# Kernel optimization log

Measured on AMD Instinct MI355X. Metric: run time of the kernel, lower is better.

## Reference

```python
import jax, jax.numpy as jnp
import numpy as np

N_NODES = 50000
N_EDGES = 800000
D = 256
N_GRAPHS = 128
N_CLASSES = 2


def gcn_conv(x, W, b, src, dst, ew):
    # PyG GCNConv: add self-loops (weight 1), symmetric norm D^-1/2 (A+I) D^-1/2, then X@W + b
    n = x.shape[0]
    deg = jax.ops.segment_sum(ew, dst, num_segments=n) + 1.0  # includes self-loop weight
    dinv = jnp.where(deg > 0, jax.lax.rsqrt(deg), 0.0)
    xw = x @ W  # [N, D_out]
    norm = dinv[src] * ew * dinv[dst]  # [E]
    msgs = xw[src] * norm[:, None]  # [E, D_out] gathered messages
    agg = jax.ops.segment_sum(msgs, dst, num_segments=n)
    agg = agg + xw * (dinv * dinv)[:, None]  # self-loop contribution
    return agg + b


def setup_inputs() -> dict:
    key = jax.random.key(0)
    ks = jax.random.split(key, 16)
    emb_x = jax.random.normal(ks[0], (N_NODES, D), dtype=jnp.float32)
    edge_index = jax.random.randint(ks[1], (2, N_EDGES), 0, N_NODES, dtype=jnp.int64)
    edge_weight = jax.random.uniform(ks[2], (N_EDGES,), dtype=jnp.float32)
    batch = jnp.sort(jax.random.randint(ks[3], (N_NODES,), 0, N_GRAPHS, dtype=jnp.int64))
    s = 1.0 / np.sqrt(D)
    params = {}
    for i, k in enumerate(ks[4:7]):
        params[f"W{i+1}"] = jax.random.normal(k, (D, D), dtype=jnp.float32) * s
        params[f"b{i+1}"] = jnp.zeros((D,), dtype=jnp.float32)
    params["fc1_w"] = jax.random.normal(ks[7], (2 * D, D), dtype=jnp.float32) / np.sqrt(2 * D)
    params["fc1_b"] = jnp.zeros((D,), dtype=jnp.float32)
    params["fc2_w"] = jax.random.normal(ks[8], (D, N_CLASSES), dtype=jnp.float32) * s
    params["fc2_b"] = jnp.zeros((N_CLASSES,), dtype=jnp.float32)
    return dict(emb_x=emb_x, edge_index=edge_index, edge_weight=edge_weight, batch=batch, **params)


def reference(emb_x, edge_index, edge_weight, batch, W1, b1, W2, b2, W3, b3, fc1_w, fc1_b, fc2_w, fc2_b):
    src, dst = edge_index[0], edge_index[1]
    x = emb_x
    for W, b in ((W1, b1), (W2, b2), (W3, b3)):
        x = gcn_conv(x, W, b, src, dst, edge_weight)
        x = jax.nn.relu(x)  # dropout is identity in eval mode
    counts = jax.ops.segment_sum(jnp.ones((x.shape[0],), x.dtype), batch, num_segments=N_GRAPHS)
    mean_x = jax.ops.segment_sum(x, batch, num_segments=N_GRAPHS) / jnp.maximum(counts, 1.0)[:, None]
    max_x = jax.ops.segment_max(x, batch, num_segments=N_GRAPHS)
    max_x = jnp.where(jnp.isfinite(max_x), max_x, 0.0)  # empty segments -> 0
    h = jnp.concatenate([mean_x, max_x], axis=1)  # [G, 2D]
    h = jax.nn.relu(h @ fc1_w + fc1_b)
    return h @ fc2_w + fc2_b  # [G, n_classes]
```

## Files before the change

kernel.cpp:

```cpp
#include <hip/hip_runtime.h>
#include <math.h>

#define N_NODES 50000
#define N_PAD 50048
#define N_EDGES 800000
#define DIM 256
#define N_GRAPHS 128

using f32x4 = __attribute__((ext_vector_type(4))) float;
using s16x8 = __attribute__((ext_vector_type(8))) short;

__device__ __forceinline__ ushort bf16_hi(float f) {
  unsigned u = __float_as_uint(f);
  return (ushort)((u + 0x7FFFu + ((u >> 16) & 1u)) >> 16);
}
__device__ __forceinline__ float bf16_up(ushort h) {
  return __uint_as_float(((unsigned)h) << 16);
}
__device__ __forceinline__ void bf16_split(float f, ushort& hh, ushort& ll) {
  hh = bf16_hi(f);
  float d = f - bf16_up(hh);
  ll = bf16_hi(d);
}

__global__ __launch_bounds__(256) void count_kernel(
    const int* __restrict__ dst, int* __restrict__ counts,
    int* __restrict__ p_local) {
  int e = blockIdx.x * 256 + threadIdx.x;
  if (e < N_EDGES) p_local[e] = atomicAdd(&counts[dst[e]], 1);
}

#define SCAN_CHUNK 1024
#define SCAN_BLOCKS ((N_NODES + SCAN_CHUNK - 1) / SCAN_CHUNK)

__global__ __launch_bounds__(256) void scan_phaseA(
    const int* __restrict__ counts, int* __restrict__ blockSums) {
  __shared__ int sdata[256];
  int b = blockIdx.x, t = threadIdx.x;
  int base = b * SCAN_CHUNK + t * 4;
  int s = 0;
#pragma unroll
  for (int i = 0; i < 4; ++i) {
    int idx = base + i;
    if (idx < N_NODES) s += counts[idx];
  }
  sdata[t] = s;
  __syncthreads();
  for (int off = 128; off > 0; off >>= 1) {
    if (t < off) sdata[t] += sdata[t + off];
    __syncthreads();
  }
  if (t == 0) blockSums[b] = sdata[0];
}

__global__ void scan_phaseB(int* __restrict__ blockSums, int* __restrict__ rs) {
  if (threadIdx.x == 0 && blockIdx.x == 0) {
    int acc = 0;
    for (int i = 0; i < SCAN_BLOCKS; ++i) {
      int v = blockSums[i];
      blockSums[i] = acc;
      acc += v;
    }
    rs[N_NODES] = acc;
  }
}

__global__ __launch_bounds__(256) void scan_phaseC(
    const int* __restrict__ counts, const int* __restrict__ blockSums,
    int* __restrict__ rs) {
  __shared__ int sdata[256];
  int b = blockIdx.x, t = threadIdx.x;
  int base = b * SCAN_CHUNK + t * 4;
  int v[4];
  int s = 0;
#pragma unroll
  for (int i = 0; i < 4; ++i) {
    int idx = base + i;
    v[i] = (idx < N_NODES) ? counts[idx] : 0;
    s += v[i];
  }
  sdata[t] = s;
  __syncthreads();
  for (int off = 1; off < 256; off <<= 1) {
    int x = (t >= off) ? sdata[t - off] : 0;
    __syncthreads();
    sdata[t] += x;
    __syncthreads();
  }
  int excl = (t == 0) ? 0 : sdata[t - 1];
  int o = blockSums[b] + excl;
#pragma unroll
  for (int i = 0; i < 4; ++i) {
    int idx = base + i;
    if (idx < N_NODES) rs[idx] = o;
    o += v[i];
  }
}

__global__ __launch_bounds__(256) void fill_kernel(
    const int* __restrict__ src, const int* __restrict__ dst,
    const float* __restrict__ ew, const int* __restrict__ rs,
    const int* __restrict__ p_local,
    int* __restrict__ csrc, float* __restrict__ cw) {
  int e = blockIdx.x * 256 + threadIdx.x;
  if (e < N_EDGES) {
    int d = dst[e];
    int pos = rs[d] + p_local[e];
    csrc[pos] = src[e];
    cw[pos] = ew[e];
  }
}

__global__ __launch_bounds__(256) void degsum_kernel(
    const int* __restrict__ rs, const float* __restrict__ cw,
    float* __restrict__ dinv) {
  int n = blockIdx.x * 256 + threadIdx.x;
  if (n >= N_NODES) return;
  int b = rs[n], e = rs[n + 1];
  float s = 1.0f;
  for (int i = b; i < e; ++i) s += cw[i];
  dinv[n] = 1.0f / sqrtf(s);
}

__global__ __launch_bounds__(256) void norm_kernel(
    const int* __restrict__ csrc, const float* __restrict__ dinv,
    float* __restrict__ cw) {
  int e = blockIdx.x * 256 + threadIdx.x;
  if (e < N_EDGES) cw[e] = cw[e] * dinv[csrc[e]];
}

__global__ __launch_bounds__(256) void round_x_kernel(
    const float* __restrict__ x, ushort* __restrict__ tab, int n4) {
  int i = blockIdx.x * 256 + threadIdx.x;
  if (i >= n4) return;
  float4 v = ((const float4*)x)[i];
  ushort4 h;
  h.x = bf16_hi(v.x);
  h.y = bf16_hi(v.y);
  h.z = bf16_hi(v.z);
  h.w = bf16_hi(v.w);
  ((ushort4*)tab)[i] = h;
}

__global__ __launch_bounds__(256) void prep_w_kernel(
    const float* __restrict__ W1, const float* __restrict__ W2, const float* __restrict__ W3,
    ushort* __restrict__ wt) {
  int k = blockIdx.x;
  int w = blockIdx.y;
  int n = threadIdx.x;
  const float* W = (w == 0) ? W1 : (w == 1) ? W2 : W3;
  float v = W[k * 256 + n];
  ushort h, l;
  bf16_split(v, h, l);
  ushort* hplane = wt + (size_t)w * 2 * 256 * 256;
  ushort* lplane = hplane + 256 * 256;
  hplane[n * 256 + k] = h;
  lplane[n * 256 + k] = l;
}

#define GBM 64
#define GBK 32

__device__ __forceinline__ void gload16(const void* g, void* l) {
  __builtin_amdgcn_global_load_lds(
      (const __attribute__((address_space(1))) void*)g,
      (__attribute__((address_space(3))) void*)l, 16, 0, 0);
}

__global__ __launch_bounds__(256) void gemm_mfma(
    const ushort* __restrict__ A,
    const ushort* __restrict__ Wh, const ushort* __restrict__ Wl,
    ushort* __restrict__ C, int M) {
  __shared__ ushort Asl[2][GBM * GBK];
  int tid = threadIdx.x;
  int bm = blockIdx.x * GBM;
  int wave = tid >> 6, lane = tid & 63;
  int wc = wave * 64;
  int l15 = lane & 15;
  int lkb = lane >> 4;

  f32x4 acc[4][4];
#pragma unroll
  for (int i = 0; i < 4; ++i)
#pragma unroll
    for (int j = 0; j < 4; ++j) acc[i][j] = (f32x4){0.f, 0.f, 0.f, 0.f};

  int arow = tid & 63, akb = tid >> 6;

#define STAGE_A(buf, ts)                                                       \
  gload16(A + (size_t)(bm + arow) * 256 + (ts) * 32 + akb * 8,                 \
          &Asl[buf][tid * 8])

  STAGE_A(0, 0);
  s16x8 bh_c[4], bl_c[4], bh_n[4], bl_n[4];
#pragma unroll
  for (int f = 0; f < 4; ++f) {
    size_t woff = (size_t)(wc + f * 16 + l15) * 256 + lkb * 8;
    bh_c[f] = *(const s16x8*)(Wh + woff);
    bl_c[f] = *(const s16x8*)(Wl + woff);
  }
  __syncthreads();
#pragma unroll
  for (int t = 0; t < 8; ++t) {
    if (t < 7) {
      STAGE_A((t & 1) ^ 1, t + 1);
#pragma unroll
      for (int f = 0; f < 4; ++f) {
        size_t woff = (size_t)(wc + f * 16 + l15) * 256 + (t + 1) * 32 + lkb * 8;
        bh_n[f] = *(const s16x8*)(Wh + woff);
        bl_n[f] = *(const s16x8*)(Wl + woff);
      }
    }
    s16x8 af[4];
#pragma unroll
    for (int f = 0; f < 4; ++f)
      af[f] = *(const s16x8*)(&Asl[t & 1][(lkb * 64 + f * 16 + l15) * 8]);
#pragma unroll
    for (int i = 0; i < 4; ++i)
#pragma unroll
      for (int j = 0; j < 4; ++j) {
        acc[i][j] = __builtin_amdgcn_mfma_f32_16x16x32_bf16(af[i], bh_c[j], acc[i][j], 0, 0, 0);
        acc[i][j] = __builtin_amdgcn_mfma_f32_16x16x32_bf16(af[i], bl_c[j], acc[i][j], 0, 0, 0);
      }
    __syncthreads();
#pragma unroll
    for (int f = 0; f < 4; ++f) { bh_c[f] = bh_n[f]; bl_c[f] = bl_n[f]; }
  }
#undef STAGE_A

#pragma unroll
  for (int i = 0; i < 4; ++i) {
    int rbase = bm + i * 16 + (lane >> 4) * 4;
#pragma unroll
    for (int j = 0; j < 4; ++j) {
      int col = wc + j * 16 + l15;
#pragma unroll
      for (int r = 0; r < 4; ++r) {
        int row = rbase + r;
        if (row < M) C[(size_t)row * 256 + col] = bf16_hi(acc[i][j][r]);
      }
    }
  }
}

template <int MODE>
__global__ __launch_bounds__(256) void spmm_row16(
    const ushort* __restrict__ xw, const int* __restrict__ rs,
    const int* __restrict__ csrc, const float* __restrict__ cw,
    const float* __restrict__ dinv, const float* __restrict__ bias,
    float* __restrict__ xf32, ushort* __restrict__ xout) {
  int wave = threadIdx.x >> 6, lane = threadIdx.x & 63;
  int n = __builtin_amdgcn_readfirstlane(blockIdx.x * 4 + wave);
  int e2 = lane >> 5;
  int c = lane & 31;
  const ushort* chunk = xw + c * 8;
  float acc[8] = {};
  int beg = __builtin_amdgcn_readfirstlane(rs[n]);
  int end = __builtin_amdgcn_readfirstlane(rs[n + 1]);
  int i = beg;
  for (; i + 8 <= end; i += 8) {
    int idx[4];
    float w[4];
    s16x8 v[4];
#pragma unroll
    for (int u = 0; u < 4; ++u) {
      idx[u] = csrc[i + 2 * u + e2];
      w[u] = cw[i + 2 * u + e2];
    }
#pragma unroll
    for (int u = 0; u < 4; ++u) v[u] = *(const s16x8*)(chunk + (size_t)idx[u] * 256);
#pragma unroll
    for (int u = 0; u < 4; ++u)
#pragma unroll
      for (int j = 0; j < 8; ++j) acc[j] += w[u] * bf16_up((ushort)v[u][j]);
  }
  for (; i < end; i += 2) {
    int ii = i + e2;
    float w = (ii < end) ? cw[ii] : 0.f;
    int id = csrc[(ii < end) ? ii : (end - 1)];
    s16x8 v = *(const s16x8*)(chunk + (size_t)id * 256);
#pragma unroll
    for (int j = 0; j < 8; ++j) acc[j] += w * bf16_up((ushort)v[j]);
  }
#pragma unroll
  for (int j = 0; j < 8; ++j) acc[j] += __shfl_xor(acc[j], 32);
  if (e2 == 0) {
    float di = dinv[n];
    float dd = di * di;
    s16x8 sv = *(const s16x8*)(chunk + (size_t)n * 256);
    int d0 = c * 8;
    const float4* bb = (const float4*)(bias + d0);
    float4 b0 = bb[0], b1 = bb[1];
    float r[8];
#pragma unroll
    for (int j = 0; j < 8; ++j) r[j] = di * acc[j] + dd * bf16_up((ushort)sv[j]);
    r[0] = fmaxf(r[0] + b0.x, 0.f);
    r[1] = fmaxf(r[1] + b0.y, 0.f);
    r[2] = fmaxf(r[2] + b0.z, 0.f);
    r[3] = fmaxf(r[3] + b0.w, 0.f);
    r[4] = fmaxf(r[4] + b1.x, 0.f);
    r[5] = fmaxf(r[5] + b1.y, 0.f);
    r[6] = fmaxf(r[6] + b1.z, 0.f);
    r[7] = fmaxf(r[7] + b1.w, 0.f);
    if (MODE == 1) {
      float4 a0, a1;
      a0.x = r[0]; a0.y = r[1]; a0.z = r[2]; a0.w = r[3];
      a1.x = r[4]; a1.y = r[5]; a1.z = r[6]; a1.w = r[7];
      float* p = xf32 + (size_t)n * 256 + d0;
      *(float4*)p = a0;
      *(float4*)(p + 4) = a1;
    } else {
      s16x8 hv;
#pragma unroll
      for (int j = 0; j < 8; ++j) hv[j] = (short)bf16_hi(r[j]);
      *(s16x8*)(xout + (size_t)n * 256 + d0) = hv;
    }
  }
}

__device__ __forceinline__ int lower_bound_dev(const int* a, int n, int key) {
  int lo = 0, hi = n;
  while (lo < hi) {
    int mid = (lo + hi) >> 1;
    if (a[mid] < key) lo = mid + 1; else hi = mid;
  }
  return lo;
}

__global__ __launch_bounds__(256) void pool_kernel(
    const float* __restrict__ x, const int* __restrict__ batch,
    float* __restrict__ h) {
  int g = blockIdx.x;
  int dchunk = blockIdx.y;
  int t = threadIdx.x;
  int dl = t & 63;
  int nl = t >> 6;
  int d = dchunk * 64 + dl;
  int start = lower_bound_dev(batch, N_NODES, g);
  int end = lower_bound_dev(batch, N_NODES, g + 1);
  float sum = 0.f, mx = 0.f;
  for (int i = start + nl; i < end; i += 4) {
    float v = x[(size_t)i * DIM + d];
    sum += v;
    mx = fmaxf(mx, v);
  }
  __shared__ float ssum[4][64];
  __shared__ float smax[4][64];
  ssum[nl][dl] = sum;
  smax[nl][dl] = mx;
  __syncthreads();
  if (nl == 0) {
    sum = ssum[0][dl] + ssum[1][dl] + ssum[2][dl] + ssum[3][dl];
    mx = fmaxf(fmaxf(smax[0][dl], smax[1][dl]), fmaxf(smax[2][dl], smax[3][dl]));
    float cnt = (float)(end - start);
    h[(size_t)g * (2 * DIM) + d] = sum / fmaxf(cnt, 1.0f);
    h[(size_t)g * (2 * DIM) + DIM + d] = mx;
  }
}

__global__ __launch_bounds__(256) void fc_kernel(
    const float* __restrict__ h, const float* __restrict__ fc1_w,
    const float* __restrict__ fc1_b, const float* __restrict__ fc2_w,
    const float* __restrict__ fc2_b, float* __restrict__ out) {
  int g = blockIdx.x;
  int j = threadIdx.x;
  __shared__ float hs[2 * DIM];
  __shared__ float s0[256], s1[256];
  hs[j] = h[(size_t)g * (2 * DIM) + j];
  hs[j + 256] = h[(size_t)g * (2 * DIM) + 256 + j];
  __syncthreads();
  float acc = fc1_b[j];
  for (int k = 0; k < 2 * DIM; ++k) acc += hs[k] * fc1_w[(size_t)k * DIM + j];
  float r = fmaxf(acc, 0.0f);
  s0[j] = r * fc2_w[j * 2 + 0];
  s1[j] = r * fc2_w[j * 2 + 1];
  __syncthreads();
  for (int off = 128; off > 0; off >>= 1) {
    if (j < off) { s0[j] += s0[j + off]; s1[j] += s1[j + off]; }
    __syncthreads();
  }
  if (j == 0) {
    out[g * 2 + 0] = s0[0] + fc2_b[0];
    out[g * 2 + 1] = s1[0] + fc2_b[1];
  }
}

extern "C" void kernel_launch(void* const* d_in, const int* in_sizes, int n_in,
                              void* d_out, int out_size, void* d_ws, size_t ws_size,
                              hipStream_t stream) {
  const float* emb_x = (const float*)d_in[0];
  const int* eidx = (const int*)d_in[1];
  const int* esrc = eidx;
  const int* edst = eidx + N_EDGES;
  const float* ew = (const float*)d_in[2];
  const int* batch = (const int*)d_in[3];
  const float* W1 = (const float*)d_in[4];
  const float* b1 = (const float*)d_in[5];
  const float* W2 = (const float*)d_in[6];
  const float* b2 = (const float*)d_in[7];
  const float* W3 = (const float*)d_in[8];
  const float* b3 = (const float*)d_in[9];
  const float* fc1_w = (const float*)d_in[10];
  const float* fc1_b = (const float*)d_in[11];
  const float* fc2_w = (const float*)d_in[12];
  const float* fc2_b = (const float*)d_in[13];
  float* out = (float*)d_out;

  char* ws = (char*)d_ws;
  size_t off = 0;
  auto take = [&](size_t bytes) -> char* {
    char* p = ws + off;
    off = (off + bytes + 255) & ~(size_t)255;
    return p;
  };
  ushort* XW = (ushort*)take((size_t)N_PAD * DIM * 2);
  ushort* Xa = (ushort*)take((size_t)N_PAD * DIM * 2);
  float* Xf32 = (float*)take((size_t)N_NODES * DIM * 4);
  ushort* WT = (ushort*)take((size_t)6 * 256 * 256 * 2);
  float* dinv = (float*)take(N_NODES * 4);
  int* counts = (int*)take(N_NODES * 4);
  int* rs = (int*)take((N_NODES + 1) * 4);
  int* p_local = (int*)take(N_EDGES * 4);
  int* blockSums = (int*)take(64 * 4);
  int* csrc = (int*)take(N_EDGES * 4);
  float* cw = (float*)take(N_EDGES * 4);
  float* h = (float*)take((size_t)N_GRAPHS * 2 * DIM * 4);

  hipMemsetAsync(counts, 0, N_NODES * 4, stream);
  hipMemsetAsync(Xa + (size_t)N_NODES * DIM, 0, (size_t)(N_PAD - N_NODES) * DIM * 2, stream);

  int eblocks = (N_EDGES + 255) / 256;
  int nblocks = (N_NODES + 255) / 256;

  count_kernel<<<eblocks, 256, 0, stream>>>(edst, counts, p_local);
  scan_phaseA<<<SCAN_BLOCKS, 256, 0, stream>>>(counts, blockSums);
  scan_phaseB<<<1, 64, 0, stream>>>(blockSums, rs);
  scan_phaseC<<<SCAN_BLOCKS, 256, 0, stream>>>(counts, blockSums, rs);
  fill_kernel<<<eblocks, 256, 0, stream>>>(esrc, edst, ew, rs, p_local, csrc, cw);
  degsum_kernel<<<nblocks, 256, 0, stream>>>(rs, cw, dinv);
  norm_kernel<<<eblocks, 256, 0, stream>>>(csrc, dinv, cw);

  round_x_kernel<<<(N_NODES * DIM / 4 + 255) / 256, 256, 0, stream>>>(
      emb_x, Xa, N_NODES * DIM / 4);
  prep_w_kernel<<<dim3(256, 3), 256, 0, stream>>>(W1, W2, W3, WT);

  ushort* W1h = WT + 0 * 65536; ushort* W1l = WT + 1 * 65536;
  ushort* W2h = WT + 2 * 65536; ushort* W2l = WT + 3 * 65536;
  ushort* W3h = WT + 4 * 65536; ushort* W3l = WT + 5 * 65536;

  dim3 ggrid(N_PAD / GBM);
  int sgrid = N_NODES / 4;

  gemm_mfma<<<ggrid, 256, 0, stream>>>(Xa, W1h, W1l, XW, N_NODES);
  spmm_row16<0><<<sgrid, 256, 0, stream>>>(XW, rs, csrc, cw, dinv, b1, nullptr, Xa);
  gemm_mfma<<<ggrid, 256, 0, stream>>>(Xa, W2h, W2l, XW, N_NODES);
  spmm_row16<0><<<sgrid, 256, 0, stream>>>(XW, rs, csrc, cw, dinv, b2, nullptr, Xa);
  gemm_mfma<<<ggrid, 256, 0, stream>>>(Xa, W3h, W3l, XW, N_NODES);
  spmm_row16<1><<<sgrid, 256, 0, stream>>>(XW, rs, csrc, cw, dinv, b3, Xf32, nullptr);

  pool_kernel<<<dim3(N_GRAPHS, 4), 256, 0, stream>>>(Xf32, batch, h);
  fc_kernel<<<N_GRAPHS, 256, 0, stream>>>(h, fc1_w, fc1_b, fc2_w, fc2_b, out);
}
```

Measured before the change: 452.1 us.

## Partition CSR build atomics, pack edge metadata, and preload full A tile in GEMM

```diff
diff --git a/kernel.cpp b/kernel.cpp
--- a/kernel.cpp
+++ b/kernel.cpp
@@ -6,6 +6,7 @@
 #define N_EDGES 800000
 #define DIM 256
 #define N_GRAPHS 128
+#define NPART 8
 
 using f32x4 = __attribute__((ext_vector_type(4))) float;
 using s16x8 = __attribute__((ext_vector_type(8))) short;
@@ -23,11 +24,23 @@
   ll = bf16_hi(d);
 }
 
-__global__ __launch_bounds__(256) void count_kernel(
-    const int* __restrict__ dst, int* __restrict__ counts,
-    int* __restrict__ p_local) {
+__global__ __launch_bounds__(256) void count8_kernel(
+    const int* __restrict__ dst, int* __restrict__ counts8,
+    int* __restrict__ p8) {
   int e = blockIdx.x * 256 + threadIdx.x;
-  if (e < N_EDGES) p_local[e] = atomicAdd(&counts[dst[e]], 1);
+  int part = blockIdx.x & (NPART - 1);
+  if (e < N_EDGES) p8[e] = atomicAdd(&counts8[part * N_NODES + dst[e]], 1);
+}
+
+__global__ __launch_bounds__(256) void sum8_kernel(
+    const int* __restrict__ counts8, int* __restrict__ counts) {
+  int n = blockIdx.x * 256 + threadIdx.x;
+  if (n < N_NODES) {
+    int s = 0;
+#pragma unroll
+    for (int p = 0; p < NPART; ++p) s += counts8[p * N_NODES + n];
+    counts[n] = s;
+  }
 }
 
 #define SCAN_CHUNK 1024
@@ -97,36 +110,54 @@
   }
 }
 
+__global__ __launch_bounds__(256) void off8_kernel(
+    const int* __restrict__ rs, const int* __restrict__ counts8,
+    int* __restrict__ off8) {
+  int n = blockIdx.x * 256 + threadIdx.x;
+  if (n < N_NODES) {
+    int acc = rs[n];
+#pragma unroll
+    for (int p = 0; p < NPART; ++p) {
+      off8[p * N_NODES + n] = acc;
+      acc += counts8[p * N_NODES + n];
+    }
+  }
+}
+
 __global__ __launch_bounds__(256) void fill_kernel(
     const int* __restrict__ src, const int* __restrict__ dst,
-    const float* __restrict__ ew, const int* __restrict__ rs,
-    const int* __restrict__ p_local,
-    int* __restrict__ csrc, float* __restrict__ cw) {
+    const float* __restrict__ ew, const int* __restrict__ off8,
+    const int* __restrict__ p8, uint2* __restrict__ meta) {
   int e = blockIdx.x * 256 + threadIdx.x;
+  int part = blockIdx.x & (NPART - 1);
   if (e < N_EDGES) {
     int d = dst[e];
-    int pos = rs[d] + p_local[e];
-    csrc[pos] = src[e];
-    cw[pos] = ew[e];
+    int pos = off8[part * N_NODES + d] + p8[e];
+    uint2 m;
+    m.x = (unsigned)src[e];
+    m.y = __float_as_uint(ew[e]);
+    meta[pos] = m;
   }
 }
 
 __global__ __launch_bounds__(256) void degsum_kernel(
-    const int* __restrict__ rs, const float* __restrict__ cw,
+    const int* __restrict__ rs, const uint2* __restrict__ meta,
     float* __restrict__ dinv) {
   int n = blockIdx.x * 256 + threadIdx.x;
   if (n >= N_NODES) return;
   int b = rs[n], e = rs[n + 1];
   float s = 1.0f;
-  for (int i = b; i < e; ++i) s += cw[i];
+  for (int i = b; i < e; ++i) s += __uint_as_float(meta[i].y);
   dinv[n] = 1.0f / sqrtf(s);
 }
 
 __global__ __launch_bounds__(256) void norm_kernel(
-    const int* __restrict__ csrc, const float* __restrict__ dinv,
-    float* __restrict__ cw) {
+    uint2* __restrict__ meta, const float* __restrict__ dinv) {
   int e = blockIdx.x * 256 + threadIdx.x;
-  if (e < N_EDGES) cw[e] = cw[e] * dinv[csrc[e]];
+  if (e < N_EDGES) {
+    uint2 m = meta[e];
+    meta[e].y = __float_as_uint(__uint_as_float(m.y) * dinv[m.x]);
+  }
 }
 
 __global__ __launch_bounds__(256) void round_x_kernel(
@@ -159,7 +190,6 @@
 }
 
 #define GBM 64
-#define GBK 32
 
 __device__ __forceinline__ void gload16(const void* g, void* l) {
   __builtin_amdgcn_global_load_lds(
@@ -171,7 +201,7 @@
     const ushort* __restrict__ A,
     const ushort* __restrict__ Wh, const ushort* __restrict__ Wl,
     ushort* __restrict__ C, int M) {
-  __shared__ ushort Asl[2][GBM * GBK];
+  __shared__ ushort Asl[GBM * 256];
   int tid = threadIdx.x;
   int bm = blockIdx.x * GBM;
   int wave = tid >> 6, lane = tid & 63;
@@ -186,12 +216,12 @@
     for (int j = 0; j < 4; ++j) acc[i][j] = (f32x4){0.f, 0.f, 0.f, 0.f};
 
   int arow = tid & 63, akb = tid >> 6;
-
-#define STAGE_A(buf, ts)                                                       \
-  gload16(A + (size_t)(bm + arow) * 256 + (ts) * 32 + akb * 8,                 \
-          &Asl[buf][tid * 8])
-
-  STAGE_A(0, 0);
+#pragma unroll
+  for (int it = 0; it < 8; ++it) {
+    gload16(A + (size_t)(bm + arow) * 256 + it * 32 + akb * 8,
+            Asl + ((it * 256 + tid) * 8));
+  }
+
   s16x8 bh_c[4], bl_c[4], bh_n[4], bl_n[4];
 #pragma unroll
   for (int f = 0; f < 4; ++f) {
@@ -200,10 +230,10 @@
     bl_c[f] = *(const s16x8*)(Wl + woff);
   }
   __syncthreads();
+
 #pragma unroll
   for (int t = 0; t < 8; ++t) {
     if (t < 7) {
-      STAGE_A((t & 1) ^ 1, t + 1);
 #pragma unroll
       for (int f = 0; f < 4; ++f) {
         size_t woff = (size_t)(wc + f * 16 + l15) * 256 + (t + 1) * 32 + lkb * 8;
@@ -214,7 +244,7 @@
     s16x8 af[4];
 #pragma unroll
     for (int f = 0; f < 4; ++f)
-      af[f] = *(const s16x8*)(&Asl[t & 1][(lkb * 64 + f * 16 + l15) * 8]);
+      af[f] = *(const s16x8*)(&Asl[(t * 256 + lkb * 64 + f * 16 + l15) * 8]);
 #pragma unroll
     for (int i = 0; i < 4; ++i)
 #pragma unroll
@@ -222,11 +252,11 @@
         acc[i][j] = __builtin_amdgcn_mfma_f32_16x16x32_bf16(af[i], bh_c[j], acc[i][j], 0, 0, 0);
         acc[i][j] = __builtin_amdgcn_mfma_f32_16x16x32_bf16(af[i], bl_c[j], acc[i][j], 0, 0, 0);
       }
-    __syncthreads();
-#pragma unroll
-    for (int f = 0; f < 4; ++f) { bh_c[f] = bh_n[f]; bl_c[f] = bl_n[f]; }
-  }
-#undef STAGE_A
+    if (t < 7) {
+#pragma unroll
+      for (int f = 0; f < 4; ++f) { bh_c[f] = bh_n[f]; bl_c[f] = bl_n[f]; }
+    }
+  }
 
 #pragma unroll
   for (int i = 0; i < 4; ++i) {
@@ -246,8 +276,8 @@
 template <int MODE>
 __global__ __launch_bounds__(256) void spmm_row16(
     const ushort* __restrict__ xw, const int* __restrict__ rs,
-    const int* __restrict__ csrc, const float* __restrict__ cw,
-    const float* __restrict__ dinv, const float* __restrict__ bias,
+    const uint2* __restrict__ meta, const float* __restrict__ dinv,
+    const float* __restrict__ bias,
     float* __restrict__ xf32, ushort* __restrict__ xout) {
   int wave = threadIdx.x >> 6, lane = threadIdx.x & 63;
   int n = __builtin_amdgcn_readfirstlane(blockIdx.x * 4 + wave);
@@ -259,26 +289,24 @@
   int end = __builtin_amdgcn_readfirstlane(rs[n + 1]);
   int i = beg;
   for (; i + 8 <= end; i += 8) {
-    int idx[4];
-    float w[4];
+    uint2 m[4];
     s16x8 v[4];
 #pragma unroll
+    for (int u = 0; u < 4; ++u) m[u] = meta[i + 2 * u + e2];
+#pragma unroll
+    for (int u = 0; u < 4; ++u) v[u] = *(const s16x8*)(chunk + (size_t)m[u].x * 256);
+#pragma unroll
     for (int u = 0; u < 4; ++u) {
-      idx[u] = csrc[i + 2 * u + e2];
-      w[u] = cw[i + 2 * u + e2];
-    }
-#pragma unroll
-    for (int u = 0; u < 4; ++u) v[u] = *(const s16x8*)(chunk + (size_t)idx[u] * 256);
-#pragma unroll
-    for (int u = 0; u < 4; ++u)
-#pragma unroll
-      for (int j = 0; j < 8; ++j) acc[j] += w[u] * bf16_up((ushort)v[u][j]);
+      float w = __uint_as_float(m[u].y);
+#pragma unroll
+      for (int j = 0; j < 8; ++j) acc[j] += w * bf16_up((ushort)v[u][j]);
+    }
   }
   for (; i < end; i += 2) {
     int ii = i + e2;
-    float w = (ii < end) ? cw[ii] : 0.f;
-    int id = csrc[(ii < end) ? ii : (end - 1)];
-    s16x8 v = *(const s16x8*)(chunk + (size_t)id * 256);
+    uint2 m = meta[(ii < end) ? ii : (end - 1)];
+    float w = (ii < end) ? __uint_as_float(m.y) : 0.f;
+    s16x8 v = *(const s16x8*)(chunk + (size_t)m.x * 256);
 #pragma unroll
     for (int j = 0; j < 8; ++j) acc[j] += w * bf16_up((ushort)v[j]);
   }
@@ -419,26 +447,29 @@
   ushort* WT = (ushort*)take((size_t)6 * 256 * 256 * 2);
   float* dinv = (float*)take(N_NODES * 4);
   int* counts = (int*)take(N_NODES * 4);
+  int* counts8 = (int*)take((size_t)NPART * N_NODES * 4);
+  int* off8 = (int*)take((size_t)NPART * N_NODES * 4);
   int* rs = (int*)take((N_NODES + 1) * 4);
-  int* p_local = (int*)take(N_EDGES * 4);
+  int* p8 = (int*)take(N_EDGES * 4);
   int* blockSums = (int*)take(64 * 4);
-  int* csrc = (int*)take(N_EDGES * 4);
-  float* cw = (float*)take(N_EDGES * 4);
+  uint2* meta = (uint2*)take((size_t)N_EDGES * 8);
   float* h = (float*)take((size_t)N_GRAPHS * 2 * DIM * 4);
 
-  hipMemsetAsync(counts, 0, N_NODES * 4, stream);
+  hipMemsetAsync(counts8, 0, (size_t)NPART * N_NODES * 4, stream);
   hipMemsetAsync(Xa + (size_t)N_NODES * DIM, 0, (size_t)(N_PAD - N_NODES) * DIM * 2, stream);
 
   int eblocks = (N_EDGES + 255) / 256;
   int nblocks = (N_NODES + 255) / 256;
 
-  count_kernel<<<eblocks, 256, 0, stream>>>(edst, counts, p_local);
+  count8_kernel<<<eblocks, 256, 0, stream>>>(edst, counts8, p8);
+  sum8_kernel<<<nblocks, 256, 0, stream>>>(counts8, counts);
   scan_phaseA<<<SCAN_BLOCKS, 256, 0, stream>>>(counts, blockSums);
   scan_phaseB<<<1, 64, 0, stream>>>(blockSums, rs);
   scan_phaseC<<<SCAN_BLOCKS, 256, 0, stream>>>(counts, blockSums, rs);
-  fill_kernel<<<eblocks, 256, 0, stream>>>(esrc, edst, ew, rs, p_local, csrc, cw);
-  degsum_kernel<<<nblocks, 256, 0, stream>>>(rs, cw, dinv);
-  norm_kernel<<<eblocks, 256, 0, stream>>>(csrc, dinv, cw);
+  off8_kernel<<<nblocks, 256, 0, stream>>>(rs, counts8, off8);
+  fill_kernel<<<eblocks, 256, 0, stream>>>(esrc, edst, ew, off8, p8, meta);
+  degsum_kernel<<<nblocks, 256, 0, stream>>>(rs, meta, dinv);
+  norm_kernel<<<eblocks, 256, 0, stream>>>(meta, dinv);
 
   round_x_kernel<<<(N_NODES * DIM / 4 + 255) / 256, 256, 0, stream>>>(
       emb_x, Xa, N_NODES * DIM / 4);
@@ -452,11 +483,11 @@
   int sgrid = N_NODES / 4;
 
   gemm_mfma<<<ggrid, 256, 0, stream>>>(Xa, W1h, W1l, XW, N_NODES);
-  spmm_row16<0><<<sgrid, 256, 0, stream>>>(XW, rs, csrc, cw, dinv, b1, nullptr, Xa);
+  spmm_row16<0><<<sgrid, 256, 0, stream>>>(XW, rs, meta, dinv, b1, nullptr, Xa);
   gemm_mfma<<<ggrid, 256, 0, stream>>>(Xa, W2h, W2l, XW, N_NODES);
-  spmm_row16<0><<<sgrid, 256, 0, stream>>>(XW, rs, csrc, cw, dinv, b2, nullptr, Xa);
+  spmm_row16<0><<<sgrid, 256, 0, stream>>>(XW, rs, meta, dinv, b2, nullptr, Xa);
   gemm_mfma<<<ggrid, 256, 0, stream>>>(Xa, W3h, W3l, XW, N_NODES);
-  spmm_row16<1><<<sgrid, 256, 0, stream>>>(XW, rs, csrc, cw, dinv, b3, Xf32, nullptr);
+  spmm_row16<1><<<sgrid, 256, 0, stream>>>(XW, rs, meta, dinv, b3, Xf32, nullptr);
 
   pool_kernel<<<dim3(N_GRAPHS, 4), 256, 0, stream>>>(Xf32, batch, h);
   fc_kernel<<<N_GRAPHS, 256, 0, stream>>>(h, fc1_w, fc1_b, fc2_w, fc2_b, out);
```

Result: no change. 448.9 us (-0.7%).
